# Optimization experiments

Measured on AMD Instinct MI355X. Metric: run time of the kernel, lower is better.

The kernel has to match this reference:

```python
import jax, jax.numpy as jnp
import numpy as np

B, S, D, H = 2, 2048, 1024, 16
DK = D // H  # 64


def _quantum(x, W1, b1, W2, b2):
    # Stand-in for QuantumNeuralLayer: classical->quantum->classical, d_k -> d_k.
    return jnp.tanh(x @ W1 + b1) @ W2 + b2


def setup_inputs() -> dict:
    key = jax.random.key(0)
    ks = jax.random.split(key, 16)
    s = 1.0 / np.sqrt(DK)
    inp = {
        "q": jax.random.normal(ks[0], (B, S, D), dtype=jnp.float32),
        "k": jax.random.normal(ks[1], (B, S, D), dtype=jnp.float32),
        "v": jax.random.normal(ks[2], (B, S, D), dtype=jnp.float32),
    }
    names = ["q", "k", "v"]
    for i, n in enumerate(names):
        inp[f"W{n}1"] = jax.random.normal(ks[3 + 4 * i], (DK, DK), dtype=jnp.float32) * s
        inp[f"b{n}1"] = jnp.zeros((DK,), dtype=jnp.float32)
        inp[f"W{n}2"] = jax.random.normal(ks[4 + 4 * i], (DK, DK), dtype=jnp.float32) * s
        inp[f"b{n}2"] = jnp.zeros((DK,), dtype=jnp.float32)
    inp["Wo"] = jax.random.normal(ks[15], (D, D), dtype=jnp.float32) * (1.0 / np.sqrt(D))
    inp["bo"] = jnp.zeros((D,), dtype=jnp.float32)
    return inp


def reference(q, k, v, Wq1, bq1, Wq2, bq2, Wk1, bk1, Wk2, bk2,
              Wv1, bv1, Wv2, bv2, Wo, bo):
    b, s, _ = q.shape
    # split heads: [B, S, H, DK]
    qh = q.reshape(b, s, H, DK)
    kh = k.reshape(b, s, H, DK)
    vh = v.reshape(b, s, H, DK)
    # quantum per-feature transform on last dim
    qh = _quantum(qh, Wq1, bq1, Wq2, bq2)
    kh = _quantum(kh, Wk1, bk1, Wk2, bk2)
    vh = _quantum(vh, Wv1, bv1, Wv2, bv2)
    scale = 1.0 / jnp.sqrt(jnp.asarray(DK, dtype=qh.dtype))
    # scores: [B, H, S, S]
    scores = jnp.einsum("bqhd,bkhd->bhqk", qh, kh) * scale
    attn = jax.nn.softmax(scores, axis=-1)
    # context: [B, H, S, DK] -> [B, S, D]
    ctx = jnp.einsum("bhqk,bkhd->bqhd", attn, vh).reshape(b, s, D)
    return ctx @ Wo + bo
```

## Files before the change

### kernel.cpp

```cpp
#include <hip/hip_runtime.h>

#define B_ 2
#define S_ 2048
#define D_ 1024
#define H_ 16
#define DK_ 64

typedef float f32x4 __attribute__((ext_vector_type(4)));
typedef float f32x16 __attribute__((ext_vector_type(16)));
typedef short bf16x8 __attribute__((ext_vector_type(8)));

static __device__ __forceinline__ unsigned short f2bf(float f) {
  unsigned u = __float_as_uint(f);
  unsigned r = (u + 0x7FFFu + ((u >> 16) & 1u)) >> 16;
  return (unsigned short)r;
}

static __device__ __forceinline__ unsigned cvtpk_bf16(float lo, float hi) {
  unsigned r;
  asm("v_cvt_pk_bf16_f32 %0, %1, %2" : "=v"(r) : "v"(lo), "v"(hi));
  return r;
}

static __device__ __forceinline__ void load16_lds(const void* g, void* lds) {
  __builtin_amdgcn_global_load_lds(
      (const __attribute__((address_space(1))) unsigned int*)g,
      (__attribute__((address_space(3))) unsigned int*)lds, 16, 0, 0);
}

static __device__ __forceinline__ bf16x8 make_pa8(const float* p, int hi) {
  unsigned x1 = cvtpk_bf16(p[0], p[1]);
  unsigned x2 = cvtpk_bf16(p[2], p[3]);
  unsigned y1 = cvtpk_bf16(p[4], p[5]);
  unsigned y2 = cvtpk_bf16(p[6], p[7]);
  unsigned sx1 = (unsigned)__shfl_xor((int)x1, 32);
  unsigned sx2 = (unsigned)__shfl_xor((int)x2, 32);
  unsigned sy1 = (unsigned)__shfl_xor((int)y1, 32);
  unsigned sy2 = (unsigned)__shfl_xor((int)y2, 32);
  union {
    unsigned u[4];
    bf16x8 v;
  } pa;
  pa.u[0] = hi ? sy1 : x1;
  pa.u[1] = hi ? sy2 : x2;
  pa.u[2] = hi ? y1 : sx1;
  pa.u[3] = hi ? y2 : sx2;
  return pa.v;
}

static __device__ __forceinline__ float tanh_fast(float x) {
  float xc = fminf(fmaxf(x, -9.0f), 9.0f);
  float e = exp2f(xc * 2.88539008177792681472f);
  return (e - 1.0f) / (e + 1.0f);
}

__global__ __launch_bounds__(256) void quantum_fused(
    const float* __restrict__ xq, const float* __restrict__ xk,
    const float* __restrict__ xv,
    const float* __restrict__ Wq1, const float* __restrict__ bq1,
    const float* __restrict__ Wq2, const float* __restrict__ bq2,
    const float* __restrict__ Wk1, const float* __restrict__ bk1,
    const float* __restrict__ Wk2, const float* __restrict__ bk2,
    const float* __restrict__ Wv1, const float* __restrict__ bv1,
    const float* __restrict__ Wv2, const float* __restrict__ bv2,
    unsigned short* __restrict__ qhb, unsigned short* __restrict__ khb,
    unsigned short* __restrict__ vtb, float qscale) {
  const int tid = threadIdx.x;
  const int w = tid >> 6;
  const int l = tid & 63;
  const int lq = l & 31;
  const int hi = l >> 5;
  const int bh = blockIdx.y;
  const int b = bh >> 4, h = bh & 15;
  const int s0w = blockIdx.x * 128 + w * 32;

  const float* x;
  const float* W1;
  const float* b1;
  const float* W2;
  const float* b2;
  unsigned short* outp;
  float scale = 1.0f;
  int vmode = 0;
  if (blockIdx.z == 0) {
    x = xq; W1 = Wq1; b1 = bq1; W2 = Wq2; b2 = bq2; outp = qhb;
    scale = qscale;
  } else if (blockIdx.z == 1) {
    x = xk; W1 = Wk1; b1 = bk1; W2 = Wk2; b2 = bk2; outp = khb;
  } else {
    x = xv; W1 = Wv1; b1 = bv1; W2 = Wv2; b2 = bv2; outp = vtb;
    vmode = 1;
  }

  bf16x8 w1f[2][4];
#pragma unroll
  for (int ca = 0; ca < 2; ++ca)
#pragma unroll
    for (int kc = 0; kc < 4; ++kc) {
      const float* wp = W1 + (size_t)(kc * 16 + hi * 8) * 64 + ca * 32 + lq;
      union {
        unsigned u[4];
        bf16x8 v;
      } ww;
#pragma unroll
      for (int jj = 0; jj < 4; ++jj)
        ww.u[jj] = cvtpk_bf16(wp[(2 * jj) * 64], wp[(2 * jj + 1) * 64]);
      w1f[ca][kc] = ww.v;
    }

  const float* xrow = x + (((size_t)b * S_ + s0w + lq) * H_ + h) * DK_;
  bf16x8 xf[4];
#pragma unroll
  for (int kc = 0; kc < 4; ++kc) {
    float4 f0 = *(const float4*)(xrow + kc * 16 + hi * 8);
    float4 f1 = *(const float4*)(xrow + kc * 16 + hi * 8 + 4);
    union {
      unsigned u[4];
      bf16x8 v;
    } xx;
    xx.u[0] = cvtpk_bf16(f0.x, f0.y);
    xx.u[1] = cvtpk_bf16(f0.z, f0.w);
    xx.u[2] = cvtpk_bf16(f1.x, f1.y);
    xx.u[3] = cvtpk_bf16(f1.z, f1.w);
    xf[kc] = xx.v;
  }

  f32x16 acc1[2];
#pragma unroll
  for (int ca = 0; ca < 2; ++ca)
#pragma unroll
    for (int r = 0; r < 16; ++r)
      acc1[ca][r] = b1[ca * 32 + (r & 3) + 8 * (r >> 2) + 4 * hi];
#pragma unroll
  for (int kc = 0; kc < 4; ++kc) {
    acc1[0] = __builtin_amdgcn_mfma_f32_32x32x16_bf16(w1f[0][kc], xf[kc], acc1[0], 0, 0, 0);
    acc1[1] = __builtin_amdgcn_mfma_f32_32x32x16_bf16(w1f[1][kc], xf[kc], acc1[1], 0, 0, 0);
  }

  float t0[16], t1[16];
#pragma unroll
  for (int r = 0; r < 16; ++r) {
    t0[r] = tanh_fast(acc1[0][r]);
    t1[r] = tanh_fast(acc1[1][r]);
  }

  bf16x8 af[4];
  af[0] = make_pa8(&t0[0], hi);
  af[1] = make_pa8(&t0[8], hi);
  af[2] = make_pa8(&t1[0], hi);
  af[3] = make_pa8(&t1[8], hi);

  bf16x8 w2f[2][4];
#pragma unroll
  for (int nb = 0; nb < 2; ++nb)
#pragma unroll
    for (int kc = 0; kc < 4; ++kc) {
      const float* wp = W2 + (size_t)(kc * 16 + hi * 8) * 64 + nb * 32 + lq;
      union {
        unsigned u[4];
        bf16x8 v;
      } ww;
#pragma unroll
      for (int jj = 0; jj < 4; ++jj)
        ww.u[jj] = cvtpk_bf16(wp[(2 * jj) * 64], wp[(2 * jj + 1) * 64]);
      w2f[nb][kc] = ww.v;
    }

  f32x16 acc2[2];
#pragma unroll
  for (int nb = 0; nb < 2; ++nb)
#pragma unroll
    for (int r = 0; r < 16; ++r)
      acc2[nb][r] = b2[nb * 32 + (r & 3) + 8 * (r >> 2) + 4 * hi];
#pragma unroll
  for (int kc = 0; kc < 4; ++kc) {
    acc2[0] = __builtin_amdgcn_mfma_f32_32x32x16_bf16(af[kc], w2f[0][kc], acc2[0], 0, 0, 0);
    acc2[1] = __builtin_amdgcn_mfma_f32_32x32x16_bf16(af[kc], w2f[1][kc], acc2[1], 0, 0, 0);
  }

  if (!vmode) {
#pragma unroll
    for (int nb = 0; nb < 2; ++nb)
#pragma unroll
      for (int r = 0; r < 16; ++r) {
        const int s = s0w + (r & 3) + 8 * (r >> 2) + 4 * hi;
        outp[((size_t)bh * S_ + s) * DK_ + nb * 32 + lq] =
            f2bf(acc2[nb][r] * scale);
      }
  } else {
#pragma unroll
    for (int nb = 0; nb < 2; ++nb) {
      float yv[16];
#pragma unroll
      for (int r = 0; r < 16; ++r) yv[r] = acc2[nb][r];
      const size_t rowb = ((size_t)bh * DK_ + nb * 32 + lq) * S_;
      *(bf16x8*)(outp + rowb + s0w + hi * 8) = make_pa8(&yv[0], hi);
      *(bf16x8*)(outp + rowb + s0w + 16 + hi * 8) = make_pa8(&yv[8], hi);
    }
  }
}

__global__ __launch_bounds__(256) void attn_kernel(
    const unsigned short* __restrict__ qhb,
    const unsigned short* __restrict__ khb,
    const unsigned short* __restrict__ vtb,
    unsigned short* __restrict__ ctxb) {
  __shared__ __align__(16) unsigned short ks_u[3][64 * 64];
  __shared__ __align__(16) unsigned short vs_u[3][64 * 64];

  const int tid = threadIdx.x;
  const int w = tid >> 6;
  const int l = tid & 63;
  const int lq = l & 31;
  const int hi = l >> 5;
  const int bh = blockIdx.x;
  const int b = bh >> 4, h = bh & 15;
  const int q0 = blockIdx.y * 128 + w * 32;

  const unsigned short* qp = qhb + ((size_t)bh * S_ + q0 + lq) * DK_ + hi * 8;
  bf16x8 qf[4];
#pragma unroll
  for (int kc = 0; kc < 4; ++kc) qf[kc] = *(const bf16x8*)(qp + kc * 16);

  f32x16 o0 = {}, o1 = {};
  float m_ = -1e30f, l_ = 0.f;

  const unsigned short* kgbase = khb + (size_t)bh * S_ * DK_;
  const unsigned short* vgbase = vtb + (size_t)bh * DK_ * S_;
  const int r0 = w * 16 + (l >> 3);
  const int sl8 = ((l & 7) ^ (l >> 3)) * 8;

#define STAGE(BUF, TT)                                                        \
  {                                                                           \
    const int tb = (TT)*64;                                                   \
    char* kb = (char*)ks_u[BUF] + w * 2048;                                   \
    char* vb = (char*)vs_u[BUF] + w * 2048;                                   \
    load16_lds(kgbase + (size_t)(tb + r0) * DK_ + sl8, kb);                   \
    load16_lds(kgbase + (size_t)(tb + r0 + 8) * DK_ + sl8, kb + 1024);        \
    load16_lds(vgbase + (size_t)r0 * S_ + tb + sl8, vb);                      \
    load16_lds(vgbase + (size_t)(r0 + 8) * S_ + tb + sl8, vb + 1024);         \
  }

  STAGE(0, 0)
  STAGE(1, 1)

  for (int t = 0; t < 32; ++t) {
    if (t < 31) {
      asm volatile("s_waitcnt vmcnt(4)" ::: "memory");
    } else {
      asm volatile("s_waitcnt vmcnt(0)" ::: "memory");
    }
    __builtin_amdgcn_sched_barrier(0);
    __builtin_amdgcn_s_barrier();
    __builtin_amdgcn_sched_barrier(0);

    const int cur = t % 3;
    const char* ksP = (const char*)ks_u[cur];
    const char* vsP = (const char*)vs_u[cur];
    if (t < 30) STAGE((t + 2) % 3, t + 2)

    f32x16 s0 = {}, s1 = {};
    __builtin_amdgcn_s_setprio(1);
#pragma unroll
    for (int kc = 0; kc < 4; ++kc) {
      const int slot = kc * 2 + hi;
      bf16x8 k0 = *(const bf16x8*)(ksP + lq * 128 + ((slot ^ (lq & 7)) << 4));
      bf16x8 k1 = *(const bf16x8*)(ksP + (32 + lq) * 128 + ((slot ^ (lq & 7)) << 4));
      s0 = __builtin_amdgcn_mfma_f32_32x32x16_bf16(k0, qf[kc], s0, 0, 0, 0);
      s1 = __builtin_amdgcn_mfma_f32_32x32x16_bf16(k1, qf[kc], s1, 0, 0, 0);
    }
    __builtin_amdgcn_s_setprio(0);

    float pmax = fmaxf(fmaxf(s0[0], s0[1]), fmaxf(s0[2], s0[3]));
#pragma unroll
    for (int i = 4; i < 16; i += 4)
      pmax = fmaxf(pmax, fmaxf(fmaxf(s0[i], s0[i + 1]), fmaxf(s0[i + 2], s0[i + 3])));
#pragma unroll
    for (int i = 0; i < 16; i += 4)
      pmax = fmaxf(pmax, fmaxf(fmaxf(s1[i], s1[i + 1]), fmaxf(s1[i + 2], s1[i + 3])));
    pmax = fmaxf(pmax, __shfl_xor(pmax, 32));

    if (!__all(pmax <= m_ + 8.0f)) {
      const float mnew = fmaxf(m_, pmax);
      const float scl = exp2f(m_ - mnew);
      m_ = mnew;
      l_ *= scl;
#pragma unroll
      for (int r = 0; r < 16; ++r) {
        const float sr = __shfl(scl, ((r & 3) + 8 * (r >> 2)) + 4 * hi);
        o0[r] *= sr;
        o1[r] *= sr;
      }
    }

#pragma unroll
    for (int i = 0; i < 16; ++i) s0[i] = exp2f(s0[i] - m_);
#pragma unroll
    for (int i = 0; i < 16; ++i) s1[i] = exp2f(s1[i] - m_);
    {
      float t0a = 0.f, t1a = 0.f, t2a = 0.f, t3a = 0.f;
#pragma unroll
      for (int i = 0; i < 16; i += 4) {
        t0a += s0[i] + s1[i];
        t1a += s0[i + 1] + s1[i + 1];
        t2a += s0[i + 2] + s1[i + 2];
        t3a += s0[i + 3] + s1[i + 3];
      }
      float ps = (t0a + t1a) + (t2a + t3a);
      ps += __shfl_xor(ps, 32);
      l_ += ps;
    }

    float pv[8];
    union {
      unsigned u[4];
      bf16x8 v;
    } pa;

#define PV_STEP(SARR, CC, CIDX)                                               \
  {                                                                           \
    _Pragma("unroll") for (int j = 0; j < 8; ++j) pv[j] = SARR[(CC)*8 + j];   \
    pa.v = make_pa8(pv, hi);                                                  \
    const int slot = (CIDX)*2 + hi;                                           \
    bf16x8 v0 = *(const bf16x8*)(vsP + lq * 128 + ((slot ^ (lq & 7)) << 4));  \
    bf16x8 v1 = *(const bf16x8*)(vsP + (32 + lq) * 128 + ((slot ^ (lq & 7)) << 4)); \
    o0 = __builtin_amdgcn_mfma_f32_32x32x16_bf16(pa.v, v0, o0, 0, 0, 0);      \
    o1 = __builtin_amdgcn_mfma_f32_32x32x16_bf16(pa.v, v1, o1, 0, 0, 0);      \
  }

    __builtin_amdgcn_s_setprio(1);
    PV_STEP(s0, 0, 0)
    PV_STEP(s0, 1, 1)
    PV_STEP(s1, 0, 2)
    PV_STEP(s1, 1, 3)
    __builtin_amdgcn_s_setprio(0);
#undef PV_STEP
  }
#undef STAGE

  const float linv = 1.0f / l_;
#pragma unroll
  for (int r = 0; r < 16; ++r) {
    const int crow = ((r & 3) + 8 * (r >> 2)) + 4 * hi;
    const float lr = __shfl(linv, crow);
    const int qg = q0 + crow;
    const size_t base = ((size_t)b * S_ + qg) * D_ + h * DK_;
    ctxb[base + lq] = f2bf(o0[r] * lr);
    ctxb[base + 32 + lq] = f2bf(o1[r] * lr);
  }
}

__global__ __launch_bounds__(256) void wo_transpose(
    const float* __restrict__ Wo, unsigned short* __restrict__ WoT) {
  __shared__ float t[64][65];
  const int k0 = blockIdx.x * 64, n0 = blockIdx.y * 64;
  const int r = threadIdx.x >> 4, c4 = threadIdx.x & 15;
#pragma unroll
  for (int i = 0; i < 4; ++i) {
    float4 v = *(const float4*)&Wo[(size_t)(k0 + r + 16 * i) * D_ + n0 + c4 * 4];
    t[r + 16 * i][c4 * 4 + 0] = v.x;
    t[r + 16 * i][c4 * 4 + 1] = v.y;
    t[r + 16 * i][c4 * 4 + 2] = v.z;
    t[r + 16 * i][c4 * 4 + 3] = v.w;
  }
  __syncthreads();
  const int n = threadIdx.x >> 2, kc = threadIdx.x & 3;
  union {
    unsigned short u[16];
    uint4 v[2];
  } pk;
#pragma unroll
  for (int j = 0; j < 16; ++j) pk.u[j] = f2bf(t[kc * 16 + j][n]);
  unsigned short* op = WoT + (size_t)(n0 + n) * D_ + k0 + kc * 16;
  *(uint4*)op = pk.v[0];
  *(uint4*)(op + 8) = pk.v[1];
}

__global__ __launch_bounds__(256) void out_gemm_mfma(
    const unsigned short* __restrict__ A,
    const unsigned short* __restrict__ BT,
    const float* __restrict__ bo, float* __restrict__ C) {
  __shared__ __align__(16) unsigned short As[3][128 * 64];
  __shared__ __align__(16) unsigned short Bs[3][128 * 64];

  const int tid = threadIdx.x;
  const int w = tid >> 6, l = tid & 63;
  const int ll = l & 15, lg = l >> 4;
  const int wr = w >> 1, wc = w & 1;
  const int m0 = blockIdx.y * 128, n0 = blockIdx.x * 128;

  const int srow = l >> 3;
  const int sslot = (l & 7) ^ srow;
  const int g_off = sslot * 8;

  f32x4 acc[4][4];
#pragma unroll
  for (int mt = 0; mt < 4; ++mt)
#pragma unroll
    for (int nt = 0; nt < 4; ++nt) acc[mt][nt] = (f32x4){0.f, 0.f, 0.f, 0.f};

#define STAGE_G(BUF, KT)                                                      \
  {                                                                           \
    const int k0e = (KT)*64;                                                  \
    _Pragma("unroll") for (int c = 0; c < 4; ++c) {                           \
      const int row = c * 32 + w * 8 + srow;                                  \
      load16_lds(A + (size_t)(m0 + row) * D_ + k0e + g_off,                   \
                 (char*)As[BUF] + c * 4096 + w * 1024);                       \
      load16_lds(BT + (size_t)(n0 + row) * D_ + k0e + g_off,                  \
                 (char*)Bs[BUF] + c * 4096 + w * 1024);                       \
    }                                                                         \
  }

  STAGE_G(0, 0)
  STAGE_G(1, 1)

  for (int kt = 0; kt < 16; ++kt) {
    if (kt < 15) {
      asm volatile("s_waitcnt vmcnt(8)" ::: "memory");
    } else {
      asm volatile("s_waitcnt vmcnt(0)" ::: "memory");
    }
    __builtin_amdgcn_sched_barrier(0);
    __builtin_amdgcn_s_barrier();
    __builtin_amdgcn_sched_barrier(0);

    const int cur = kt % 3;
    if (kt < 14) STAGE_G((kt + 2) % 3, kt + 2)

#pragma unroll
    for (int half = 0; half < 2; ++half) {
      bf16x8 af[4], bfr[4];
#pragma unroll
      for (int mt = 0; mt < 4; ++mt) {
        const int row = wr * 64 + mt * 16 + ll;
        af[mt] = *(const bf16x8*)((const char*)As[cur] + row * 128 +
                                  (((half * 4 + lg) ^ (row & 7)) << 4));
      }
#pragma unroll
      for (int nt = 0; nt < 4; ++nt) {
        const int rowb = wc * 64 + nt * 16 + ll;
        bfr[nt] = *(const bf16x8*)((const char*)Bs[cur] + rowb * 128 +
                                   (((half * 4 + lg) ^ (rowb & 7)) << 4));
      }
      __builtin_amdgcn_s_setprio(1);
#pragma unroll
      for (int mt = 0; mt < 4; ++mt)
#pragma unroll
        for (int nt = 0; nt < 4; ++nt)
          acc[mt][nt] = __builtin_amdgcn_mfma_f32_16x16x32_bf16(
              af[mt], bfr[nt], acc[mt][nt], 0, 0, 0);
      __builtin_amdgcn_s_setprio(0);
    }
  }
#undef STAGE_G

#pragma unroll
  for (int nt = 0; nt < 4; ++nt) {
    const int col = n0 + wc * 64 + nt * 16 + ll;
    const float bv = bo[col];
#pragma unroll
    for (int mt = 0; mt < 4; ++mt) {
      const int row0 = m0 + wr * 64 + mt * 16 + lg * 4;
#pragma unroll
      for (int r = 0; r < 4; ++r)
        C[(size_t)(row0 + r) * D_ + col] = acc[mt][nt][r] + bv;
    }
  }
}

extern "C" void kernel_launch(void* const* d_in, const int* in_sizes, int n_in,
                              void* d_out, int out_size, void* d_ws,
                              size_t ws_size, hipStream_t stream) {
  const float* q = (const float*)d_in[0];
  const float* k = (const float*)d_in[1];
  const float* v = (const float*)d_in[2];
  const float* Wq1 = (const float*)d_in[3];
  const float* bq1 = (const float*)d_in[4];
  const float* Wq2 = (const float*)d_in[5];
  const float* bq2 = (const float*)d_in[6];
  const float* Wk1 = (const float*)d_in[7];
  const float* bk1 = (const float*)d_in[8];
  const float* Wk2 = (const float*)d_in[9];
  const float* bk2 = (const float*)d_in[10];
  const float* Wv1 = (const float*)d_in[11];
  const float* bv1 = (const float*)d_in[12];
  const float* Wv2 = (const float*)d_in[13];
  const float* bv2 = (const float*)d_in[14];
  const float* Wo = (const float*)d_in[15];
  const float* bo = (const float*)d_in[16];
  float* out = (float*)d_out;

  const size_t TEN = (size_t)B_ * H_ * S_ * DK_;
  char* ws = (char*)d_ws;
  unsigned short* qhb = (unsigned short*)ws;
  unsigned short* khb = (unsigned short*)(ws + TEN * 2);
  unsigned short* vtb = (unsigned short*)(ws + TEN * 4);
  unsigned short* ctxb = (unsigned short*)(ws + TEN * 6);
  unsigned short* wot = (unsigned short*)(ws + TEN * 8);

  const float cs = 0.125f * 1.44269504088896340736f;
  quantum_fused<<<dim3(16, 32, 3), 256, 0, stream>>>(
      q, k, v, Wq1, bq1, Wq2, bq2, Wk1, bk1, Wk2, bk2, Wv1, bv1, Wv2, bv2,
      qhb, khb, vtb, cs);
  wo_transpose<<<dim3(16, 16), 256, 0, stream>>>(Wo, wot);

  attn_kernel<<<dim3(32, 16), 256, 0, stream>>>(qhb, khb, vtb, ctxb);

  out_gemm_mfma<<<dim3(8, 32), 256, 0, stream>>>(ctxb, wot, bo, out);
}
```

Baseline: 116.1 us.

## Split attention KV tile across wave pairs and merge partial softmax results

```diff
diff --git a/kernel.cpp b/kernel.cpp
--- a/kernel.cpp
+++ b/kernel.cpp
@@ -200,22 +200,23 @@
   }
 }
 
-__global__ __launch_bounds__(256) void attn_kernel(
+__global__ __launch_bounds__(256, 4) void attn_kernel(
     const unsigned short* __restrict__ qhb,
     const unsigned short* __restrict__ khb,
     const unsigned short* __restrict__ vtb,
     unsigned short* __restrict__ ctxb) {
-  __shared__ __align__(16) unsigned short ks_u[3][64 * 64];
-  __shared__ __align__(16) unsigned short vs_u[3][64 * 64];
+  __shared__ __align__(16) unsigned short ks_u[2][64 * 64];
+  __shared__ __align__(16) unsigned short vs_u[2][64 * 64];
 
   const int tid = threadIdx.x;
   const int w = tid >> 6;
   const int l = tid & 63;
   const int lq = l & 31;
   const int hi = l >> 5;
+  const int khalf = w >> 1;
   const int bh = blockIdx.x;
   const int b = bh >> 4, h = bh & 15;
-  const int q0 = blockIdx.y * 128 + w * 32;
+  const int q0 = blockIdx.y * 64 + (w & 1) * 32;
 
   const unsigned short* qp = qhb + ((size_t)bh * S_ + q0 + lq) * DK_ + hi * 8;
   bf16x8 qf[4];
@@ -242,32 +243,22 @@
   }
 
   STAGE(0, 0)
-  STAGE(1, 1)
+  __syncthreads();
+
+  const int kr = khalf * 32 + lq;
 
   for (int t = 0; t < 32; ++t) {
-    if (t < 31) {
-      asm volatile("s_waitcnt vmcnt(4)" ::: "memory");
-    } else {
-      asm volatile("s_waitcnt vmcnt(0)" ::: "memory");
-    }
-    __builtin_amdgcn_sched_barrier(0);
-    __builtin_amdgcn_s_barrier();
-    __builtin_amdgcn_sched_barrier(0);
-
-    const int cur = t % 3;
+    const int cur = t & 1;
     const char* ksP = (const char*)ks_u[cur];
     const char* vsP = (const char*)vs_u[cur];
-    if (t < 30) STAGE((t + 2) % 3, t + 2)
-
-    f32x16 s0 = {}, s1 = {};
+    if (t < 31) STAGE(cur ^ 1, t + 1)
+
+    f32x16 s0 = {};
     __builtin_amdgcn_s_setprio(1);
 #pragma unroll
     for (int kc = 0; kc < 4; ++kc) {
-      const int slot = kc * 2 + hi;
-      bf16x8 k0 = *(const bf16x8*)(ksP + lq * 128 + ((slot ^ (lq & 7)) << 4));
-      bf16x8 k1 = *(const bf16x8*)(ksP + (32 + lq) * 128 + ((slot ^ (lq & 7)) << 4));
+      bf16x8 k0 = *(const bf16x8*)(ksP + kr * 128 + (((kc * 2 + hi) ^ (kr & 7)) << 4));
       s0 = __builtin_amdgcn_mfma_f32_32x32x16_bf16(k0, qf[kc], s0, 0, 0, 0);
-      s1 = __builtin_amdgcn_mfma_f32_32x32x16_bf16(k1, qf[kc], s1, 0, 0, 0);
     }
     __builtin_amdgcn_s_setprio(0);
 
@@ -275,9 +266,6 @@
 #pragma unroll
     for (int i = 4; i < 16; i += 4)
       pmax = fmaxf(pmax, fmaxf(fmaxf(s0[i], s0[i + 1]), fmaxf(s0[i + 2], s0[i + 3])));
-#pragma unroll
-    for (int i = 0; i < 16; i += 4)
-      pmax = fmaxf(pmax, fmaxf(fmaxf(s1[i], s1[i + 1]), fmaxf(s1[i + 2], s1[i + 3])));
     pmax = fmaxf(pmax, __shfl_xor(pmax, 32));
 
     if (!__all(pmax <= m_ + 8.0f)) {
@@ -295,58 +283,70 @@
 
 #pragma unroll
     for (int i = 0; i < 16; ++i) s0[i] = exp2f(s0[i] - m_);
-#pragma unroll
-    for (int i = 0; i < 16; ++i) s1[i] = exp2f(s1[i] - m_);
     {
-      float t0a = 0.f, t1a = 0.f, t2a = 0.f, t3a = 0.f;
-#pragma unroll
-      for (int i = 0; i < 16; i += 4) {
-        t0a += s0[i] + s1[i];
-        t1a += s0[i + 1] + s1[i + 1];
-        t2a += s0[i + 2] + s1[i + 2];
-        t3a += s0[i + 3] + s1[i + 3];
-      }
+      float t0a = (s0[0] + s0[1]) + (s0[2] + s0[3]);
+      float t1a = (s0[4] + s0[5]) + (s0[6] + s0[7]);
+      float t2a = (s0[8] + s0[9]) + (s0[10] + s0[11]);
+      float t3a = (s0[12] + s0[13]) + (s0[14] + s0[15]);
       float ps = (t0a + t1a) + (t2a + t3a);
       ps += __shfl_xor(ps, 32);
       l_ += ps;
     }
 
     float pv[8];
-    union {
-      unsigned u[4];
-      bf16x8 v;
-    } pa;
-
-#define PV_STEP(SARR, CC, CIDX)                                               \
-  {                                                                           \
-    _Pragma("unroll") for (int j = 0; j < 8; ++j) pv[j] = SARR[(CC)*8 + j];   \
-    pa.v = make_pa8(pv, hi);                                                  \
-    const int slot = (CIDX)*2 + hi;                                           \
-    bf16x8 v0 = *(const bf16x8*)(vsP + lq * 128 + ((slot ^ (lq & 7)) << 4));  \
-    bf16x8 v1 = *(const bf16x8*)(vsP + (32 + lq) * 128 + ((slot ^ (lq & 7)) << 4)); \
-    o0 = __builtin_amdgcn_mfma_f32_32x32x16_bf16(pa.v, v0, o0, 0, 0, 0);      \
-    o1 = __builtin_amdgcn_mfma_f32_32x32x16_bf16(pa.v, v1, o1, 0, 0, 0);      \
-  }
-
     __builtin_amdgcn_s_setprio(1);
-    PV_STEP(s0, 0, 0)
-    PV_STEP(s0, 1, 1)
-    PV_STEP(s1, 0, 2)
-    PV_STEP(s1, 1, 3)
+#pragma unroll
+    for (int kc = 0; kc < 2; ++kc) {
+#pragma unroll
+      for (int j = 0; j < 8; ++j) pv[j] = s0[kc * 8 + j];
+      bf16x8 pav = make_pa8(pv, hi);
+      const int slot = khalf * 4 + kc * 2 + hi;
+      bf16x8 v0 = *(const bf16x8*)(vsP + lq * 128 + ((slot ^ (lq & 7)) << 4));
+      bf16x8 v1 = *(const bf16x8*)(vsP + (32 + lq) * 128 + ((slot ^ (lq & 7)) << 4));
+      o0 = __builtin_amdgcn_mfma_f32_32x32x16_bf16(pav, v0, o0, 0, 0, 0);
+      o1 = __builtin_amdgcn_mfma_f32_32x32x16_bf16(pav, v1, o1, 0, 0, 0);
+    }
     __builtin_amdgcn_s_setprio(0);
-#undef PV_STEP
+
+    __syncthreads();
   }
 #undef STAGE
 
-  const float linv = 1.0f / l_;
-#pragma unroll
-  for (int r = 0; r < 16; ++r) {
-    const int crow = ((r & 3) + 8 * (r >> 2)) + 4 * hi;
-    const float lr = __shfl(linv, crow);
-    const int qg = q0 + crow;
-    const size_t base = ((size_t)b * S_ + qg) * D_ + h * DK_;
-    ctxb[base + lq] = f2bf(o0[r] * lr);
-    ctxb[base + 32 + lq] = f2bf(o1[r] * lr);
+  float* ksf = (float*)&ks_u[0][0];
+  float* mlf = (float*)&vs_u[0][0];
+  const int qlb = (w & 1) * 32;
+
+  if (khalf == 1) {
+#pragma unroll
+    for (int r = 0; r < 16; ++r) {
+      const int ql = qlb + (r & 3) + 8 * (r >> 2) + 4 * hi;
+      ksf[ql * 64 + lq] = o0[r];
+      ksf[ql * 64 + 32 + lq] = o1[r];
+    }
+    if (l < 32) {
+      mlf[(qlb + lq) * 2] = m_;
+      mlf[(qlb + lq) * 2 + 1] = l_;
+    }
+  }
+  __syncthreads();
+
+  if (khalf == 0) {
+    const float mB = mlf[(qlb + lq) * 2], lB = mlf[(qlb + lq) * 2 + 1];
+    const float mm = fmaxf(m_, mB);
+    const float al = exp2f(m_ - mm), be = exp2f(mB - mm);
+    const float li = 1.0f / (l_ * al + lB * be);
+    const float fa = al * li, fb = be * li;
+#pragma unroll
+    for (int r = 0; r < 16; ++r) {
+      const int crow = ((r & 3) + 8 * (r >> 2)) + 4 * hi;
+      const float fa_r = __shfl(fa, crow);
+      const float fb_r = __shfl(fb, crow);
+      const int ql = qlb + crow;
+      const int qg = blockIdx.y * 64 + ql;
+      const size_t base = ((size_t)b * S_ + qg) * D_ + h * DK_;
+      ctxb[base + lq] = f2bf(o0[r] * fa_r + ksf[ql * 64 + lq] * fb_r);
+      ctxb[base + 32 + lq] = f2bf(o1[r] * fa_r + ksf[ql * 64 + 32 + lq] * fb_r);
+    }
   }
 }
 
@@ -504,7 +504,7 @@
       qhb, khb, vtb, cs);
   wo_transpose<<<dim3(16, 16), 256, 0, stream>>>(Wo, wot);
 
-  attn_kernel<<<dim3(32, 16), 256, 0, stream>>>(qhb, khb, vtb, ctxb);
+  attn_kernel<<<dim3(32, 32), 256, 0, stream>>>(qhb, khb, vtb, ctxb);
 
   out_gemm_mfma<<<dim3(8, 32), 256, 0, stream>>>(ctxb, wot, bo, out);
 }
```

Result: slower. 118.9 us (+2.4%).
